# Optimization experiments

Measured on AMD Instinct MI355X. Metric: run time of the kernel, lower is better.

## Reference

```python
import jax, jax.numpy as jnp
import numpy as np

N = 40000      # nodes
E = 640000     # edges (before self-loops)
G = 64         # graphs in batch
H = 4          # heads
C = 64         # channels per head (graph_hidden_channels)
F_IN = 256     # num_node_features
NHID = 1024
NOUT = 768
NEG_SLOPE = 0.2


def setup_inputs() -> dict:
    key = jax.random.key(0)
    ks = jax.random.split(key, 20)
    s = 0.05
    inp = {
        "x": jax.random.normal(ks[0], (N, F_IN), jnp.float32),
        "edge_index": jax.random.randint(ks[1], (2, E), 0, N, dtype=jnp.int64),
        "batch": jnp.sort(jax.random.randint(ks[2], (N,), 0, G, dtype=jnp.int64)),
        # GATConv 1: in F_IN -> H heads x C
        "W1": jax.random.normal(ks[3], (F_IN, H * C), jnp.float32) * s,
        "as1": jax.random.normal(ks[4], (H, C), jnp.float32) * s,
        "ad1": jax.random.normal(ks[5], (H, C), jnp.float32) * s,
        "b1": jnp.zeros((H * C,), jnp.float32),
        # GATConv 2: in H*C -> H x C
        "W2": jax.random.normal(ks[6], (H * C, H * C), jnp.float32) * s,
        "as2": jax.random.normal(ks[7], (H, C), jnp.float32) * s,
        "ad2": jax.random.normal(ks[8], (H, C), jnp.float32) * s,
        "b2": jnp.zeros((H * C,), jnp.float32),
        # GATConv 3
        "W3": jax.random.normal(ks[9], (H * C, H * C), jnp.float32) * s,
        "as3": jax.random.normal(ks[10], (H, C), jnp.float32) * s,
        "ad3": jax.random.normal(ks[11], (H, C), jnp.float32) * s,
        "b3": jnp.zeros((H * C,), jnp.float32),
        # MLP head
        "Wm1": jax.random.normal(ks[12], (H * C, NHID), jnp.float32) * s,
        "bm1": jnp.zeros((NHID,), jnp.float32),
        "Wm2": jax.random.normal(ks[13], (NHID, NOUT), jnp.float32) * s,
        "bm2": jnp.zeros((NOUT,), jnp.float32),
    }
    return inp


def _gat_layer(x, src, dst, W, a_src, a_dst, b):
    """PyG GATConv (concat=True, self-loops already in src/dst)."""
    n = x.shape[0]
    h = (x @ W).reshape(n, H, C)                       # [N,H,C]
    # per-node attention scalars (gather scalars per edge, not full features)
    alpha_src = jnp.einsum('nhc,hc->nh', h, a_src)     # [N,H]
    alpha_dst = jnp.einsum('nhc,hc->nh', h, a_dst)     # [N,H]
    e = alpha_src[src] + alpha_dst[dst]                # [E,H]
    e = jax.nn.leaky_relu(e, NEG_SLOPE)
    # segment softmax over incoming edges of each dst node
    m = jax.ops.segment_max(e, dst, num_segments=n)    # [N,H]
    e = jnp.exp(e - m[dst])
    denom = jax.ops.segment_sum(e, dst, num_segments=n)  # [N,H]; >0 via self-loops
    alpha = e / denom[dst]                             # [E,H]
    # scatter-add weighted source features to destinations
    msg = h[src] * alpha[:, :, None]                   # [E,H,C]
    out = jax.ops.segment_sum(msg, dst, num_segments=n)  # [N,H,C]
    return out.reshape(n, H * C) + b


def reference(x, edge_index, batch,
              W1, as1, ad1, b1,
              W2, as2, ad2, b2,
              W3, as3, ad3, b3,
              Wm1, bm1, Wm2, bm2):
    n = x.shape[0]
    loops = jnp.arange(n, dtype=edge_index.dtype)
    src = jnp.concatenate([edge_index[0], loops])
    dst = jnp.concatenate([edge_index[1], loops])

    h = jax.nn.relu(_gat_layer(x, src, dst, W1, as1, ad1, b1))
    h = jax.nn.relu(_gat_layer(h, src, dst, W2, as2, ad2, b2))
    h = _gat_layer(h, src, dst, W3, as3, ad3, b3)

    # global mean pool over graphs
    sums = jax.ops.segment_sum(h, batch, num_segments=G)      # [G, H*C]
    counts = jax.ops.segment_sum(jnp.ones((n,), h.dtype), batch, num_segments=G)
    pooled = sums / jnp.maximum(counts, 1.0)[:, None]

    out = jax.nn.relu(pooled @ Wm1 + bm1)
    out = out @ Wm2 + bm2
    return out
```

## Files before the change

### kernel.cpp

```cpp
#include <hip/hip_runtime.h>
#include <hip/hip_bf16.h>
#include <math.h>

#define N_NODES 40000
#define N_EDGES 640000
#define N_GRAPH 64
#define HEADS 4
#define CHAN 64
#define HC 256
#define NHID 1024
#define NOUT 768
#define E_TOT (N_EDGES + N_NODES)
#define SCAN_NB ((N_NODES + 255) / 256)

typedef __attribute__((ext_vector_type(8))) short bf16x8;
typedef __attribute__((ext_vector_type(4))) float f32x4;

__device__ inline float bflo(unsigned u) { return __uint_as_float(u << 16); }
__device__ inline float bfhi(unsigned u) { return __uint_as_float(u & 0xffff0000u); }


__global__ void cast_x_kernel(const float* __restrict__ x, __hip_bfloat16* __restrict__ xb) {
    int i = blockIdx.x * blockDim.x + threadIdx.x;
    float4 v = *reinterpret_cast<const float4*>(&x[(size_t)i * 4]);
    __hip_bfloat16 o[4] = {__float2bfloat16(v.x), __float2bfloat16(v.y),
                           __float2bfloat16(v.z), __float2bfloat16(v.w)};
    *reinterpret_cast<ushort4*>(&xb[(size_t)i * 4]) = *reinterpret_cast<ushort4*>(o);
}

__global__ void conv_wt_kernel(const float* __restrict__ W, __hip_bfloat16* __restrict__ Wt) {
    int k = blockIdx.x, n = threadIdx.x;
    Wt[(size_t)n * 256 + k] = __float2bfloat16(W[(size_t)k * 256 + n]);
}


__global__ void count_deg_kernel(const int* __restrict__ ei, int* __restrict__ deg) {
    int i = blockIdx.x * blockDim.x + threadIdx.x;
    if (i >= E_TOT) return;
    int dst = (i < N_EDGES) ? ei[N_EDGES + i] : (i - N_EDGES);
    atomicAdd(&deg[dst], 1);
}


__global__ __launch_bounds__(256)
void scan_p1_kernel(const int* __restrict__ deg, int* __restrict__ bsum) {
    const int b = blockIdx.x, t = threadIdx.x;
    const int i = b * 256 + t;
    int v = (i < N_NODES) ? deg[i] : 0;
    #pragma unroll
    for (int off = 1; off < 64; off <<= 1) v += __shfl_xor(v, off, 64);
    __shared__ int ws[4];
    if ((t & 63) == 0) ws[t >> 6] = v;
    __syncthreads();
    if (t == 0) bsum[b] = ws[0] + ws[1] + ws[2] + ws[3];
}

__global__ __launch_bounds__(256)
void scan_p2_kernel(int* __restrict__ bsum) {
    __shared__ int s[256];
    const int t = threadIdx.x;
    int v = (t < SCAN_NB) ? bsum[t] : 0;
    s[t] = v;
    __syncthreads();
    #pragma unroll
    for (int off = 1; off < 256; off <<= 1) {
        int x = (t >= off) ? s[t - off] : 0;
        __syncthreads();
        s[t] += x;
        __syncthreads();
    }
    if (t < SCAN_NB) bsum[t] = s[t] - v;
}

__global__ __launch_bounds__(256)
void scan_p3_kernel(const int* __restrict__ deg, const int* __restrict__ bsum,
                    int* __restrict__ rowptr) {
    __shared__ int s[256];
    const int b = blockIdx.x, t = threadIdx.x;
    const int i = b * 256 + t;
    int v = (i < N_NODES) ? deg[i] : 0;
    s[t] = v;
    __syncthreads();
    #pragma unroll
    for (int off = 1; off < 256; off <<= 1) {
        int x = (t >= off) ? s[t - off] : 0;
        __syncthreads();
        s[t] += x;
        __syncthreads();
    }
    if (i < N_NODES) rowptr[i] = bsum[b] + s[t] - v;
    if (i == 0) rowptr[N_NODES] = E_TOT;
}

__global__ void fill_csr_kernel(const int* __restrict__ ei, const int* __restrict__ rowptr,
                                int* __restrict__ cursor, int* __restrict__ csr_src) {
    int i = blockIdx.x * blockDim.x + threadIdx.x;
    if (i >= E_TOT) return;
    int src, dst;
    if (i < N_EDGES) { src = ei[i]; dst = ei[N_EDGES + i]; }
    else             { src = dst = i - N_EDGES; }
    int pos = atomicAdd(&cursor[dst], 1);
    csr_src[rowptr[dst] + pos] = src;
}


#define GBM 128
#define GBN 128
#define GBK 32

__global__ __launch_bounds__(256)
void gemm_mfma_kernel(const __hip_bfloat16* __restrict__ A, const __hip_bfloat16* __restrict__ Wt,
                      __hip_bfloat16* __restrict__ C, int nrows,
                      const float* __restrict__ a_s, const float* __restrict__ a_d,
                      float* __restrict__ asrc, float* __restrict__ adst) {
    __shared__ ushort A_lds[128][40];
    __shared__ ushort B_lds[128][40];
    const int tid = threadIdx.x;
    const int lane = tid & 63;
    const int l15 = lane & 15;
    const int lq  = lane >> 4;
    const int wid = tid >> 6;
    const int wrow = (wid >> 1) * 64;
    const int wcol = (wid & 1) * 64;
    const int row0 = blockIdx.x * GBM;
    const int col0 = blockIdx.y * GBN;

    f32x4 acc[4][4];
    #pragma unroll
    for (int m = 0; m < 4; m++)
        #pragma unroll
        for (int n = 0; n < 4; n++)
            acc[m][n] = (f32x4){0.f, 0.f, 0.f, 0.f};

    const char* Ab = (const char*)A;
    const char* Wb = (const char*)Wt;

    for (int kt = 0; kt < 256; kt += GBK) {
        __syncthreads();
        #pragma unroll
        for (int i = 0; i < 2; i++) {
            int ch = tid + i * 256;
            int r = ch >> 2, sl = ch & 3;
            int arow = row0 + r; if (arow >= nrows) arow = nrows - 1;
            uint4 va = *reinterpret_cast<const uint4*>(Ab + (size_t)arow * 512 + kt * 2 + sl * 16);
            *reinterpret_cast<uint4*>(&A_lds[r][sl * 8]) = va;
            uint4 vb = *reinterpret_cast<const uint4*>(Wb + (size_t)(col0 + r) * 512 + kt * 2 + sl * 16);
            *reinterpret_cast<uint4*>(&B_lds[r][sl * 8]) = vb;
        }
        __syncthreads();
        bf16x8 af[4], bfr[4];
        #pragma unroll
        for (int m = 0; m < 4; m++)
            af[m] = *reinterpret_cast<const bf16x8*>(&A_lds[wrow + m * 16 + l15][lq * 8]);
        #pragma unroll
        for (int n = 0; n < 4; n++)
            bfr[n] = *reinterpret_cast<const bf16x8*>(&B_lds[wcol + n * 16 + l15][lq * 8]);
        #pragma unroll
        for (int m = 0; m < 4; m++)
            #pragma unroll
            for (int n = 0; n < 4; n++)
                acc[m][n] = __builtin_amdgcn_mfma_f32_16x16x32_bf16(af[m], bfr[n], acc[m][n], 0, 0, 0);
    }

    const int head = (col0 + wcol) >> 6;
    float was[4], wad[4];
    #pragma unroll
    for (int n = 0; n < 4; n++) {
        was[n] = a_s[head * 64 + n * 16 + l15];
        wad[n] = a_d[head * 64 + n * 16 + l15];
    }
    #pragma unroll
    for (int m = 0; m < 4; m++) {
        #pragma unroll
        for (int reg = 0; reg < 4; reg++) {
            float ps = 0.f, pd = 0.f;
            #pragma unroll
            for (int n = 0; n < 4; n++) {
                float v = acc[m][n][reg];
                ps = fmaf(v, was[n], ps);
                pd = fmaf(v, wad[n], pd);
            }
            #pragma unroll
            for (int off = 1; off < 16; off <<= 1) {
                ps += __shfl_xor(ps, off, 16);
                pd += __shfl_xor(pd, off, 16);
            }
            int row = row0 + wrow + m * 16 + lq * 4 + reg;
            if (l15 == 0 && row < nrows) {
                asrc[row * 4 + head] = ps;
                adst[row * 4 + head] = pd;
            }
        }
        #pragma unroll
        for (int n = 0; n < 4; n++) {
            int col = col0 + wcol + n * 16 + l15;
            #pragma unroll
            for (int reg = 0; reg < 4; reg++) {
                int row = row0 + wrow + m * 16 + lq * 4 + reg;
                if (row < nrows)
                    C[(size_t)row * 256 + col] = __float2bfloat16(acc[m][n][reg]);
            }
        }
    }
}


#define ACHUNK 256

__global__ __launch_bounds__(256)
void gat_fused_agg(const __hip_bfloat16* __restrict__ h, const float* __restrict__ asrc,
                   const float* __restrict__ adst, const int* __restrict__ rowptr,
                   const int* __restrict__ csr_src, const float* __restrict__ bias,
                   __hip_bfloat16* __restrict__ out, int do_relu) {
    __shared__ int   s_src[ACHUNK];
    __shared__ float s_w[ACHUNK][5];
    __shared__ float s_acc[8][HC];
    __shared__ float s_sum[4];

    const int n = blockIdx.x;
    const int t = threadIdx.x;
    const int lane = t & 63;
    const int wid = t >> 6;
    const int grp = t >> 5;
    const int gl  = t & 31;
    const int h3  = gl >> 3;
    const int start = rowptr[n];
    const int deg = rowptr[n + 1] - start;
    const float ad = adst[n * 4 + wid];

    float ssum = 0.f;
    float acc[8] = {0.f, 0.f, 0.f, 0.f, 0.f, 0.f, 0.f, 0.f};

    for (int c0 = 0; c0 < deg; c0 += ACHUNK) {
        const int cn = min(ACHUNK, deg - c0);
        if (c0) __syncthreads();
        for (int e = lane; e < cn; e += 64) {
            int src = csr_src[start + c0 + e];
            if (wid == 0) s_src[e] = src;
            float sc = asrc[src * 4 + wid] + ad;
            sc = (sc >= 0.f) ? sc : 0.2f * sc;
            float w = __expf(sc);
            s_w[e][wid] = w;
            ssum += w;
        }
        __syncthreads();
        #pragma unroll 2
        for (int e = grp; e < cn; e += 8) {
            float w = s_w[e][h3];
            uint4 v = *reinterpret_cast<const uint4*>(&h[(size_t)s_src[e] * HC + gl * 8]);
            acc[0] = fmaf(w, bflo(v.x), acc[0]);
            acc[1] = fmaf(w, bfhi(v.x), acc[1]);
            acc[2] = fmaf(w, bflo(v.y), acc[2]);
            acc[3] = fmaf(w, bfhi(v.y), acc[3]);
            acc[4] = fmaf(w, bflo(v.z), acc[4]);
            acc[5] = fmaf(w, bfhi(v.z), acc[5]);
            acc[6] = fmaf(w, bflo(v.w), acc[6]);
            acc[7] = fmaf(w, bfhi(v.w), acc[7]);
        }
    }
    #pragma unroll
    for (int off = 1; off < 64; off <<= 1) ssum += __shfl_xor(ssum, off, 64);
    if (lane == 0) s_sum[wid] = ssum;
    #pragma unroll
    for (int j = 0; j < 8; j++) s_acc[grp][gl * 8 + j] = acc[j];
    __syncthreads();
    float tot = 0.f;
    #pragma unroll
    for (int g = 0; g < 8; g++) tot += s_acc[g][t];
    float r = tot / s_sum[t >> 6] + bias[t];
    if (do_relu) r = fmaxf(r, 0.f);
    out[(size_t)n * HC + t] = __float2bfloat16(r);
}


__global__ void graph_bounds_kernel(const int* __restrict__ batch, int* __restrict__ cnt) {
    int g = threadIdx.x;
    if (g >= N_GRAPH) return;
    int lo = 0, hi = N_NODES;
    while (lo < hi) { int mid = (lo + hi) >> 1; if (batch[mid] < g) lo = mid + 1; else hi = mid; }
    int start = lo;
    lo = 0; hi = N_NODES;
    while (lo < hi) { int mid = (lo + hi) >> 1; if (batch[mid] < g + 1) lo = mid + 1; else hi = mid; }
    cnt[g] = lo - start;
}

__global__ __launch_bounds__(256)
void pool_kernel(const __hip_bfloat16* __restrict__ h, const int* __restrict__ batch,
                 float* __restrict__ pooled) {
    __shared__ float s_acc[8][HC];
    const int g = blockIdx.x;
    const int t = threadIdx.x;
    const int grp = t >> 5;
    const int gl  = t & 31;
    int lo = 0, hi = N_NODES;
    while (lo < hi) { int mid = (lo + hi) >> 1; if (batch[mid] < g) lo = mid + 1; else hi = mid; }
    const int start = lo;
    lo = 0; hi = N_NODES;
    while (lo < hi) { int mid = (lo + hi) >> 1; if (batch[mid] < g + 1) lo = mid + 1; else hi = mid; }
    const int end = lo;

    float acc[8] = {0.f, 0.f, 0.f, 0.f, 0.f, 0.f, 0.f, 0.f};
    for (int n = start + grp; n < end; n += 8) {
        uint4 v = *reinterpret_cast<const uint4*>(&h[(size_t)n * HC + gl * 8]);
        acc[0] += bflo(v.x); acc[1] += bfhi(v.x);
        acc[2] += bflo(v.y); acc[3] += bfhi(v.y);
        acc[4] += bflo(v.z); acc[5] += bfhi(v.z);
        acc[6] += bflo(v.w); acc[7] += bfhi(v.w);
    }
    #pragma unroll
    for (int j = 0; j < 8; j++) s_acc[grp][gl * 8 + j] = acc[j];
    __syncthreads();
    float tot = 0.f;
    #pragma unroll
    for (int q = 0; q < 8; q++) tot += s_acc[q][t];
    pooled[g * HC + t] = tot;
}


__global__ __launch_bounds__(1024)
void mlp1_kernel(const float* __restrict__ pooled, const int* __restrict__ cnt,
                 const float* __restrict__ W, const float* __restrict__ b,
                 float* __restrict__ hidden) {
    __shared__ float row[256];
    const int g = blockIdx.x, t = threadIdx.x;
    if (t < 256) {
        float c = (float)max(cnt[g], 1);
        row[t] = pooled[g * 256 + t] / c;
    }
    __syncthreads();
    float acc = b[t];
    for (int k = 0; k < 256; k++) acc = fmaf(row[k], W[(size_t)k * NHID + t], acc);
    hidden[g * NHID + t] = fmaxf(acc, 0.f);
}

__global__ __launch_bounds__(768)
void mlp2_kernel(const float* __restrict__ hidden, const float* __restrict__ W,
                 const float* __restrict__ b, float* __restrict__ out) {
    __shared__ float row[NHID];
    const int g = blockIdx.x, t = threadIdx.x;
    row[t] = hidden[g * NHID + t];
    if (t < NHID - NOUT) row[NOUT + t] = hidden[g * NHID + NOUT + t];
    __syncthreads();
    float acc = b[t];
    for (int k = 0; k < NHID; k++) acc = fmaf(row[k], W[(size_t)k * NOUT + t], acc);
    out[g * NOUT + t] = acc;
}


extern "C" void kernel_launch(void* const* d_in, const int* in_sizes, int n_in,
                              void* d_out, int out_size, void* d_ws, size_t ws_size,
                              hipStream_t stream) {
    const float* x  = (const float*)d_in[0];
    const int* ei   = (const int*)d_in[1];
    const int* batch = (const int*)d_in[2];
    const float* W1 = (const float*)d_in[3];
    const float* as1 = (const float*)d_in[4];
    const float* ad1 = (const float*)d_in[5];
    const float* b1 = (const float*)d_in[6];
    const float* W2 = (const float*)d_in[7];
    const float* as2 = (const float*)d_in[8];
    const float* ad2 = (const float*)d_in[9];
    const float* b2 = (const float*)d_in[10];
    const float* W3 = (const float*)d_in[11];
    const float* as3 = (const float*)d_in[12];
    const float* ad3 = (const float*)d_in[13];
    const float* b3 = (const float*)d_in[14];
    const float* Wm1 = (const float*)d_in[15];
    const float* bm1 = (const float*)d_in[16];
    const float* Wm2 = (const float*)d_in[17];
    const float* bm2 = (const float*)d_in[18];
    float* out = (float*)d_out;

    char* base = (char*)d_ws;
    size_t off = 0;
    auto alloc = [&](size_t bytes) { char* p = base + off; off = (off + bytes + 255) & ~(size_t)255; return p; };
    __hip_bfloat16* x_bf = (__hip_bfloat16*)alloc((size_t)N_NODES * 256 * 2);
    __hip_bfloat16* hA   = (__hip_bfloat16*)alloc((size_t)N_NODES * 256 * 2);
    __hip_bfloat16* hB   = (__hip_bfloat16*)alloc((size_t)N_NODES * 256 * 2);
    __hip_bfloat16* Wt1  = (__hip_bfloat16*)alloc((size_t)256 * 256 * 2);
    __hip_bfloat16* Wt2  = (__hip_bfloat16*)alloc((size_t)256 * 256 * 2);
    __hip_bfloat16* Wt3  = (__hip_bfloat16*)alloc((size_t)256 * 256 * 2);
    float* asrc   = (float*)alloc((size_t)N_NODES * 4 * 4);
    float* adst   = (float*)alloc((size_t)N_NODES * 4 * 4);
    int*   deg    = (int*)alloc((size_t)N_NODES * 4);
    int*   cursor = (int*)alloc((size_t)N_NODES * 4);
    int*   rowptr = (int*)alloc((size_t)(N_NODES + 1) * 4);
    int*   bsum   = (int*)alloc((size_t)SCAN_NB * 4);
    int*   csrsrc = (int*)alloc((size_t)E_TOT * 4);
    float* pooled = (float*)alloc((size_t)N_GRAPH * 256 * 4);
    int*   cnt    = (int*)alloc((size_t)N_GRAPH * 4);
    float* hidden = (float*)alloc((size_t)N_GRAPH * NHID * 4);
    (void)ws_size; (void)n_in; (void)in_sizes; (void)out_size;

    hipMemsetAsync(deg, 0, (size_t)N_NODES * 4, stream);
    hipMemsetAsync(cursor, 0, (size_t)N_NODES * 4, stream);

    cast_x_kernel<<<(N_NODES * 256 / 4 + 255) / 256, 256, 0, stream>>>(x, x_bf);
    conv_wt_kernel<<<256, 256, 0, stream>>>(W1, Wt1);
    conv_wt_kernel<<<256, 256, 0, stream>>>(W2, Wt2);
    conv_wt_kernel<<<256, 256, 0, stream>>>(W3, Wt3);

    const int eb = (E_TOT + 255) / 256;
    count_deg_kernel<<<eb, 256, 0, stream>>>(ei, deg);
    scan_p1_kernel<<<SCAN_NB, 256, 0, stream>>>(deg, bsum);
    scan_p2_kernel<<<1, 256, 0, stream>>>(bsum);
    scan_p3_kernel<<<SCAN_NB, 256, 0, stream>>>(deg, bsum, rowptr);
    fill_csr_kernel<<<eb, 256, 0, stream>>>(ei, rowptr, cursor, csrsrc);

    dim3 ggrid((N_NODES + GBM - 1) / GBM, 256 / GBN);

    gemm_mfma_kernel<<<ggrid, 256, 0, stream>>>(x_bf, Wt1, hA, N_NODES, as1, ad1, asrc, adst);
    gat_fused_agg<<<N_NODES, 256, 0, stream>>>(hA, asrc, adst, rowptr, csrsrc, b1, hB, 1);
    gemm_mfma_kernel<<<ggrid, 256, 0, stream>>>(hB, Wt2, hA, N_NODES, as2, ad2, asrc, adst);
    gat_fused_agg<<<N_NODES, 256, 0, stream>>>(hA, asrc, adst, rowptr, csrsrc, b2, hB, 1);
    gemm_mfma_kernel<<<ggrid, 256, 0, stream>>>(hB, Wt3, hA, N_NODES, as3, ad3, asrc, adst);
    gat_fused_agg<<<N_NODES, 256, 0, stream>>>(hA, asrc, adst, rowptr, csrsrc, b3, hB, 0);

    graph_bounds_kernel<<<1, 64, 0, stream>>>(batch, cnt);
    pool_kernel<<<N_GRAPH, 256, 0, stream>>>(hB, batch, pooled);
    mlp1_kernel<<<N_GRAPH, 1024, 0, stream>>>(pooled, cnt, Wm1, bm1, hidden);
    mlp2_kernel<<<N_GRAPH, NOUT, 0, stream>>>(hidden, Wm2, bm2, out);
}
```

Measured before the change: 417.3 us.

## Retile GAT GEMM to full-width rows with prefetch, pack FMAs in aggregation

The GEMM now has each block compute 64 full rows across all 256 columns, with one wave per head. Global loads for the next K-slice are prefetched into registers while MFMAs run on the current slice, and the epilogue goes through an LDS strip so each thread can write packed 16-byte bf16 stores and reduce the attention scalars with fewer shuffles. The aggregation inner loop uses v_pk_fma_f32 on pairs of channels, and the three weight-transpose launches are merged into one. The risks are that the 64-row tile drops the row-bounds guard, so it depends on N being divisible by 64, and that occupancy may fall because of the larger LDS footprint.

```diff
diff --git a/kernel.cpp b/kernel.cpp
--- a/kernel.cpp
+++ b/kernel.cpp
@@ -15,9 +15,25 @@
 
 typedef __attribute__((ext_vector_type(8))) short bf16x8;
 typedef __attribute__((ext_vector_type(4))) float f32x4;
+typedef __attribute__((ext_vector_type(2))) float f32x2;
 
 __device__ inline float bflo(unsigned u) { return __uint_as_float(u << 16); }
 __device__ inline float bfhi(unsigned u) { return __uint_as_float(u & 0xffff0000u); }
+
+__device__ inline f32x2 unpk2(unsigned u) {
+    return (f32x2){__uint_as_float(u << 16), __uint_as_float(u & 0xffff0000u)};
+}
+__device__ inline void pkfma(f32x2& a, f32x2 w2, f32x2 h2) {
+    asm("v_pk_fma_f32 %0, %1, %2, %0" : "+v"(a) : "v"(w2), "v"(h2));
+}
+
+__device__ inline unsigned bfbits(float f) {
+    __hip_bfloat16 b = __float2bfloat16(f);
+    return (unsigned)*reinterpret_cast<unsigned short*>(&b);
+}
+__device__ inline unsigned pk2bf(float lo, float hi) {
+    return bfbits(lo) | (bfbits(hi) << 16);
+}
 
 
 __global__ void cast_x_kernel(const float* __restrict__ x, __hip_bfloat16* __restrict__ xb) {
@@ -28,9 +44,13 @@
     *reinterpret_cast<ushort4*>(&xb[(size_t)i * 4]) = *reinterpret_cast<ushort4*>(o);
 }
 
-__global__ void conv_wt_kernel(const float* __restrict__ W, __hip_bfloat16* __restrict__ Wt) {
+__global__ void conv_wt3_kernel(const float* __restrict__ W1, const float* __restrict__ W2,
+                                const float* __restrict__ W3, __hip_bfloat16* __restrict__ T1,
+                                __hip_bfloat16* __restrict__ T2, __hip_bfloat16* __restrict__ T3) {
+    const float* W = (blockIdx.y == 0) ? W1 : (blockIdx.y == 1) ? W2 : W3;
+    __hip_bfloat16* T = (blockIdx.y == 0) ? T1 : (blockIdx.y == 1) ? T2 : T3;
     int k = blockIdx.x, n = threadIdx.x;
-    Wt[(size_t)n * 256 + k] = __float2bfloat16(W[(size_t)k * 256 + n]);
+    T[(size_t)n * 256 + k] = __float2bfloat16(W[(size_t)k * 256 + n]);
 }
 
 
@@ -40,7 +60,6 @@
     int dst = (i < N_EDGES) ? ei[N_EDGES + i] : (i - N_EDGES);
     atomicAdd(&deg[dst], 1);
 }
-
 
 __global__ __launch_bounds__(256)
 void scan_p1_kernel(const int* __restrict__ deg, int* __restrict__ bsum) {
@@ -104,26 +123,29 @@
 }
 
 
-#define GBM 128
-#define GBN 128
-#define GBK 32
-
 __global__ __launch_bounds__(256)
 void gemm_mfma_kernel(const __hip_bfloat16* __restrict__ A, const __hip_bfloat16* __restrict__ Wt,
-                      __hip_bfloat16* __restrict__ C, int nrows,
+                      __hip_bfloat16* __restrict__ C,
                       const float* __restrict__ a_s, const float* __restrict__ a_d,
                       float* __restrict__ asrc, float* __restrict__ adst) {
-    __shared__ ushort A_lds[128][40];
-    __shared__ ushort B_lds[128][40];
+    __shared__ __align__(16) union {
+        struct { ushort A[64][40]; ushort B[256][40]; } t;
+        float strip[4][16][68];
+    } lds;
+
     const int tid = threadIdx.x;
     const int lane = tid & 63;
     const int l15 = lane & 15;
     const int lq  = lane >> 4;
-    const int wid = tid >> 6;
-    const int wrow = (wid >> 1) * 64;
-    const int wcol = (wid & 1) * 64;
-    const int row0 = blockIdx.x * GBM;
-    const int col0 = blockIdx.y * GBN;
+    const int wc  = tid >> 6;
+    const int row0 = blockIdx.x * 64;
+
+    const char* Ab = (const char*)A;
+    const char* Wb = (const char*)Wt;
+
+    const int ar = tid >> 2;
+    const int aq = tid & 3;
+    const size_t a_goff = (size_t)(row0 + ar) * 512 + aq * 16;
 
     f32x4 acc[4][4];
     #pragma unroll
@@ -132,75 +154,91 @@
         for (int n = 0; n < 4; n++)
             acc[m][n] = (f32x4){0.f, 0.f, 0.f, 0.f};
 
-    const char* Ab = (const char*)A;
-    const char* Wb = (const char*)Wt;
-
-    for (int kt = 0; kt < 256; kt += GBK) {
-        __syncthreads();
-        #pragma unroll
-        for (int i = 0; i < 2; i++) {
-            int ch = tid + i * 256;
-            int r = ch >> 2, sl = ch & 3;
-            int arow = row0 + r; if (arow >= nrows) arow = nrows - 1;
-            uint4 va = *reinterpret_cast<const uint4*>(Ab + (size_t)arow * 512 + kt * 2 + sl * 16);
-            *reinterpret_cast<uint4*>(&A_lds[r][sl * 8]) = va;
-            uint4 vb = *reinterpret_cast<const uint4*>(Wb + (size_t)(col0 + r) * 512 + kt * 2 + sl * 16);
-            *reinterpret_cast<uint4*>(&B_lds[r][sl * 8]) = vb;
-        }
-        __syncthreads();
+    uint4 ra, rb0, rb1, rb2, rb3;
+    ra  = *reinterpret_cast<const uint4*>(Ab + a_goff);
+    rb0 = *reinterpret_cast<const uint4*>(Wb + (size_t)(ar      ) * 512 + aq * 16);
+    rb1 = *reinterpret_cast<const uint4*>(Wb + (size_t)(ar +  64) * 512 + aq * 16);
+    rb2 = *reinterpret_cast<const uint4*>(Wb + (size_t)(ar + 128) * 512 + aq * 16);
+    rb3 = *reinterpret_cast<const uint4*>(Wb + (size_t)(ar + 192) * 512 + aq * 16);
+    *reinterpret_cast<uint4*>(&lds.t.A[ar][aq * 8]) = ra;
+    *reinterpret_cast<uint4*>(&lds.t.B[ar][aq * 8]) = rb0;
+    *reinterpret_cast<uint4*>(&lds.t.B[ar + 64][aq * 8]) = rb1;
+    *reinterpret_cast<uint4*>(&lds.t.B[ar + 128][aq * 8]) = rb2;
+    *reinterpret_cast<uint4*>(&lds.t.B[ar + 192][aq * 8]) = rb3;
+    __syncthreads();
+
+    for (int kt = 0; kt < 8; ++kt) {
+        if (kt < 7) {
+            const size_t ko = (size_t)(kt + 1) * 64;
+            ra  = *reinterpret_cast<const uint4*>(Ab + a_goff + ko);
+            rb0 = *reinterpret_cast<const uint4*>(Wb + (size_t)(ar      ) * 512 + aq * 16 + ko);
+            rb1 = *reinterpret_cast<const uint4*>(Wb + (size_t)(ar +  64) * 512 + aq * 16 + ko);
+            rb2 = *reinterpret_cast<const uint4*>(Wb + (size_t)(ar + 128) * 512 + aq * 16 + ko);
+            rb3 = *reinterpret_cast<const uint4*>(Wb + (size_t)(ar + 192) * 512 + aq * 16 + ko);
+        }
         bf16x8 af[4], bfr[4];
         #pragma unroll
         for (int m = 0; m < 4; m++)
-            af[m] = *reinterpret_cast<const bf16x8*>(&A_lds[wrow + m * 16 + l15][lq * 8]);
+            af[m] = *reinterpret_cast<const bf16x8*>(&lds.t.A[m * 16 + l15][lq * 8]);
         #pragma unroll
         for (int n = 0; n < 4; n++)
-            bfr[n] = *reinterpret_cast<const bf16x8*>(&B_lds[wcol + n * 16 + l15][lq * 8]);
+            bfr[n] = *reinterpret_cast<const bf16x8*>(&lds.t.B[wc * 64 + n * 16 + l15][lq * 8]);
         #pragma unroll
         for (int m = 0; m < 4; m++)
             #pragma unroll
             for (int n = 0; n < 4; n++)
                 acc[m][n] = __builtin_amdgcn_mfma_f32_16x16x32_bf16(af[m], bfr[n], acc[m][n], 0, 0, 0);
-    }
-
-    const int head = (col0 + wcol) >> 6;
-    float was[4], wad[4];
-    #pragma unroll
-    for (int n = 0; n < 4; n++) {
-        was[n] = a_s[head * 64 + n * 16 + l15];
-        wad[n] = a_d[head * 64 + n * 16 + l15];
-    }
+        __syncthreads();
+        if (kt < 7) {
+            *reinterpret_cast<uint4*>(&lds.t.A[ar][aq * 8]) = ra;
+            *reinterpret_cast<uint4*>(&lds.t.B[ar][aq * 8]) = rb0;
+            *reinterpret_cast<uint4*>(&lds.t.B[ar + 64][aq * 8]) = rb1;
+            *reinterpret_cast<uint4*>(&lds.t.B[ar + 128][aq * 8]) = rb2;
+            *reinterpret_cast<uint4*>(&lds.t.B[ar + 192][aq * 8]) = rb3;
+            __syncthreads();
+        }
+    }
+
+    const int head = wc;
+    const int r  = lane >> 2;
+    const int cq = lane & 3;
     #pragma unroll
     for (int m = 0; m < 4; m++) {
         #pragma unroll
-        for (int reg = 0; reg < 4; reg++) {
-            float ps = 0.f, pd = 0.f;
+        for (int n = 0; n < 4; n++)
             #pragma unroll
-            for (int n = 0; n < 4; n++) {
-                float v = acc[m][n][reg];
-                ps = fmaf(v, was[n], ps);
-                pd = fmaf(v, wad[n], pd);
+            for (int reg = 0; reg < 4; reg++)
+                lds.strip[wc][lq * 4 + reg][n * 16 + l15] = acc[m][n][reg];
+        f32x4 c0 = *reinterpret_cast<const f32x4*>(&lds.strip[wc][r][cq * 16]);
+        f32x4 c1 = *reinterpret_cast<const f32x4*>(&lds.strip[wc][r][cq * 16 + 4]);
+        f32x4 c2 = *reinterpret_cast<const f32x4*>(&lds.strip[wc][r][cq * 16 + 8]);
+        f32x4 c3 = *reinterpret_cast<const f32x4*>(&lds.strip[wc][r][cq * 16 + 12]);
+        float ps = 0.f, pd = 0.f;
+        #pragma unroll
+        for (int k4 = 0; k4 < 4; k4++) {
+            f32x4 cv = (k4 == 0) ? c0 : (k4 == 1) ? c1 : (k4 == 2) ? c2 : c3;
+            #pragma unroll
+            for (int j = 0; j < 4; j++) {
+                float wsv = a_s[head * 64 + cq * 16 + k4 * 4 + j];
+                float wdv = a_d[head * 64 + cq * 16 + k4 * 4 + j];
+                ps = fmaf(cv[j], wsv, ps);
+                pd = fmaf(cv[j], wdv, pd);
             }
-            #pragma unroll
-            for (int off = 1; off < 16; off <<= 1) {
-                ps += __shfl_xor(ps, off, 16);
-                pd += __shfl_xor(pd, off, 16);
-            }
-            int row = row0 + wrow + m * 16 + lq * 4 + reg;
-            if (l15 == 0 && row < nrows) {
-                asrc[row * 4 + head] = ps;
-                adst[row * 4 + head] = pd;
-            }
-        }
-        #pragma unroll
-        for (int n = 0; n < 4; n++) {
-            int col = col0 + wcol + n * 16 + l15;
-            #pragma unroll
-            for (int reg = 0; reg < 4; reg++) {
-                int row = row0 + wrow + m * 16 + lq * 4 + reg;
-                if (row < nrows)
-                    C[(size_t)row * 256 + col] = __float2bfloat16(acc[m][n][reg]);
-            }
-        }
+        }
+        ps += __shfl_xor(ps, 1, 4); ps += __shfl_xor(ps, 2, 4);
+        pd += __shfl_xor(pd, 1, 4); pd += __shfl_xor(pd, 2, 4);
+        const int row = row0 + m * 16 + r;
+        if (cq == 0) {
+            asrc[row * 4 + head] = ps;
+            adst[row * 4 + head] = pd;
+        }
+        uint4 o0 = make_uint4(pk2bf(c0[0], c0[1]), pk2bf(c0[2], c0[3]),
+                              pk2bf(c1[0], c1[1]), pk2bf(c1[2], c1[3]));
+        uint4 o1 = make_uint4(pk2bf(c2[0], c2[1]), pk2bf(c2[2], c2[3]),
+                              pk2bf(c3[0], c3[1]), pk2bf(c3[2], c3[3]));
+        __hip_bfloat16* Cp = C + (size_t)row * 256 + wc * 64 + cq * 16;
+        *reinterpret_cast<uint4*>(Cp) = o0;
+        *reinterpret_cast<uint4*>(Cp + 8) = o1;
     }
 }
 
@@ -229,7 +267,7 @@
     const float ad = adst[n * 4 + wid];
 
     float ssum = 0.f;
-    float acc[8] = {0.f, 0.f, 0.f, 0.f, 0.f, 0.f, 0.f, 0.f};
+    f32x2 ap0 = {0.f, 0.f}, ap1 = {0.f, 0.f}, ap2 = {0.f, 0.f}, ap3 = {0.f, 0.f};
 
     for (int c0 = 0; c0 < deg; c0 += ACHUNK) {
         const int cn = min(ACHUNK, deg - c0);
@@ -247,22 +285,21 @@
         #pragma unroll 2
         for (int e = grp; e < cn; e += 8) {
             float w = s_w[e][h3];
+            f32x2 w2 = {w, w};
             uint4 v = *reinterpret_cast<const uint4*>(&h[(size_t)s_src[e] * HC + gl * 8]);
-            acc[0] = fmaf(w, bflo(v.x), acc[0]);
-            acc[1] = fmaf(w, bfhi(v.x), acc[1]);
-            acc[2] = fmaf(w, bflo(v.y), acc[2]);
-            acc[3] = fmaf(w, bfhi(v.y), acc[3]);
-            acc[4] = fmaf(w, bflo(v.z), acc[4]);
-            acc[5] = fmaf(w, bfhi(v.z), acc[5]);
-            acc[6] = fmaf(w, bflo(v.w), acc[6]);
-            acc[7] = fmaf(w, bfhi(v.w), acc[7]);
+            pkfma(ap0, w2, unpk2(v.x));
+            pkfma(ap1, w2, unpk2(v.y));
+            pkfma(ap2, w2, unpk2(v.z));
+            pkfma(ap3, w2, unpk2(v.w));
         }
     }
     #pragma unroll
     for (int off = 1; off < 64; off <<= 1) ssum += __shfl_xor(ssum, off, 64);
     if (lane == 0) s_sum[wid] = ssum;
-    #pragma unroll
-    for (int j = 0; j < 8; j++) s_acc[grp][gl * 8 + j] = acc[j];
+    s_acc[grp][gl * 8 + 0] = ap0.x; s_acc[grp][gl * 8 + 1] = ap0.y;
+    s_acc[grp][gl * 8 + 2] = ap1.x; s_acc[grp][gl * 8 + 3] = ap1.y;
+    s_acc[grp][gl * 8 + 4] = ap2.x; s_acc[grp][gl * 8 + 5] = ap2.y;
+    s_acc[grp][gl * 8 + 6] = ap3.x; s_acc[grp][gl * 8 + 7] = ap3.y;
     __syncthreads();
     float tot = 0.f;
     #pragma unroll
@@ -396,9 +433,7 @@
     hipMemsetAsync(cursor, 0, (size_t)N_NODES * 4, stream);
 
     cast_x_kernel<<<(N_NODES * 256 / 4 + 255) / 256, 256, 0, stream>>>(x, x_bf);
-    conv_wt_kernel<<<256, 256, 0, stream>>>(W1, Wt1);
-    conv_wt_kernel<<<256, 256, 0, stream>>>(W2, Wt2);
-    conv_wt_kernel<<<256, 256, 0, stream>>>(W3, Wt3);
+    conv_wt3_kernel<<<dim3(256, 3), 256, 0, stream>>>(W1, W2, W3, Wt1, Wt2, Wt3);
 
     const int eb = (E_TOT + 255) / 256;
     count_deg_kernel<<<eb, 256, 0, stream>>>(ei, deg);
@@ -407,13 +442,13 @@
     scan_p3_kernel<<<SCAN_NB, 256, 0, stream>>>(deg, bsum, rowptr);
     fill_csr_kernel<<<eb, 256, 0, stream>>>(ei, rowptr, cursor, csrsrc);
 
-    dim3 ggrid((N_NODES + GBM - 1) / GBM, 256 / GBN);
-
-    gemm_mfma_kernel<<<ggrid, 256, 0, stream>>>(x_bf, Wt1, hA, N_NODES, as1, ad1, asrc, adst);
+    const int ggrid = N_NODES / 64;
+
+    gemm_mfma_kernel<<<ggrid, 256, 0, stream>>>(x_bf, Wt1, hA, as1, ad1, asrc, adst);
     gat_fused_agg<<<N_NODES, 256, 0, stream>>>(hA, asrc, adst, rowptr, csrsrc, b1, hB, 1);
-    gemm_mfma_kernel<<<ggrid, 256, 0, stream>>>(hB, Wt2, hA, N_NODES, as2, ad2, asrc, adst);
+    gemm_mfma_kernel<<<ggrid, 256, 0, stream>>>(hB, Wt2, hA, as2, ad2, asrc, adst);
     gat_fused_agg<<<N_NODES, 256, 0, stream>>>(hA, asrc, adst, rowptr, csrsrc, b2, hB, 1);
-    gemm_mfma_kernel<<<ggrid, 256, 0, stream>>>(hB, Wt3, hA, N_NODES, as3, ad3, asrc, adst);
+    gemm_mfma_kernel<<<ggrid, 256, 0, stream>>>(hB, Wt3, hA, as3, ad3, asrc, adst);
     gat_fused_agg<<<N_NODES, 256, 0, stream>>>(hA, asrc, adst, rowptr, csrsrc, b3, hB, 0);
 
     graph_bounds_kernel<<<1, 64, 0, stream>>>(batch, cnt);
```

New measurement: 432.9 us. 1.04x slower.
